# Optimization experiments

Hardware: AMD Instinct MI355X
Metric: run time of the kernel (lower is better)

## Reference

```python
import jax, jax.numpy as jnp
import numpy as np

T, B = 21, 4096
H, E, V = 1024, 50, 96
PAD = 0


def setup_inputs() -> dict:
    key = jax.random.key(0)
    ks = jax.random.split(key, 10)
    s_e = 1.0 / np.sqrt(H)  # torch LSTM init scale
    emb = jax.random.normal(ks[0], (V, E), jnp.float32)
    emb = emb.at[PAD].set(0.0)  # padding_idx row is zero
    return {
        "input_ids": jax.random.randint(ks[1], (T, B), 0, V),
        "h0": jax.random.normal(ks[2], (1, B, H), jnp.float32),
        "c0": jax.random.normal(ks[3], (1, B, H), jnp.float32),
        "emb": emb,
        "W_ih": jax.random.uniform(ks[4], (4 * H, E), jnp.float32, -s_e, s_e),
        "W_hh": jax.random.uniform(ks[5], (4 * H, H), jnp.float32, -s_e, s_e),
        "b_ih": jax.random.uniform(ks[6], (4 * H,), jnp.float32, -s_e, s_e),
        "b_hh": jax.random.uniform(ks[7], (4 * H,), jnp.float32, -s_e, s_e),
        "W_out": jax.random.uniform(ks[8], (V, H), jnp.float32, -s_e, s_e),
        "b_out": jax.random.uniform(ks[9], (V,), jnp.float32, -s_e, s_e),
    }


def reference(input_ids, h0, c0, emb, W_ih, W_hh, b_ih, b_hh, W_out, b_out):
    # char_embeds: (T, B, E)
    x = emb[input_ids]
    # Precompute input projections for all timesteps in one GEMM: (T, B, 4H)
    x_proj = jnp.einsum("tbe,ge->tbg", x, W_ih) + b_ih + b_hh

    def step(carry, xp_t):
        h, c = carry  # (B, H) each
        gates = xp_t + h @ W_hh.T  # (B, 4H), torch gate order i,f,g,o
        i, f, g, o = jnp.split(gates, 4, axis=-1)
        i = jax.nn.sigmoid(i)
        f = jax.nn.sigmoid(f)
        g = jnp.tanh(g)
        o = jax.nn.sigmoid(o)
        c = f * c + i * g
        h = o * jnp.tanh(c)
        return (h, c), h

    (h_T, c_T), h_ts = jax.lax.scan(step, (h0[0], c0[0]), x_proj)
    # char_output_projection: (T, B, V)
    scores = jnp.einsum("tbh,vh->tbv", h_ts, W_out) + b_out
    return scores, (h_T[None], c_T[None])
```

## Files before the change

kernel.cpp:

```cpp
#include <hip/hip_runtime.h>
#include <hip/hip_bf16.h>


#define T_STEPS 21
#define BSZ 4096
#define HDIM 1024
#define VOCAB 96
#define EDIM 50

typedef __attribute__((ext_vector_type(8))) short short8;
typedef __attribute__((ext_vector_type(4))) short shortx4;
typedef __attribute__((ext_vector_type(4))) float f32x4;

#define GLL16(g, l)                                                        \
  __builtin_amdgcn_global_load_lds(                                        \
      (const __attribute__((address_space(1))) void*)(g),                  \
      (__attribute__((address_space(3))) void*)(l), 16, 0, 0)

#define ASM_BARRIER() asm volatile("s_barrier" ::: "memory")
#define ASM_VMCNT3() asm volatile("s_waitcnt vmcnt(3)" ::: "memory")
#define ASM_VMCNT0() asm volatile("s_waitcnt vmcnt(0)" ::: "memory")

__device__ __forceinline__ float sigmoidf_fast(float x) {
  return 1.0f / (1.0f + __expf(-x));
}
__device__ __forceinline__ float tanhf_fast(float x) {
  return 2.0f / (1.0f + __expf(-2.0f * x)) - 1.0f;
}
__device__ __forceinline__ float b2f(short s) {
  return __uint_as_float(((unsigned int)(unsigned short)s) << 16);
}

__global__ void prep_convert(const float* __restrict__ Whh_f,
                             const float* __restrict__ Wout_f,
                             const float* __restrict__ h0,
                             __hip_bfloat16* __restrict__ Whh,
                             __hip_bfloat16* __restrict__ Wout,
                             __hip_bfloat16* __restrict__ hb0) {
  int idx = blockIdx.x * 256 + threadIdx.x;
  if (idx < 4 * HDIM * HDIM) {
    Whh[idx] = __float2bfloat16(Whh_f[idx]);
    hb0[idx] = __float2bfloat16(h0[idx]);
  }
  if (idx < VOCAB * HDIM) Wout[idx] = __float2bfloat16(Wout_f[idx]);
}

__global__ void prep_ptable(const float* __restrict__ emb,
                            const float* __restrict__ Wih,
                            const float* __restrict__ bih,
                            const float* __restrict__ bhh,
                            __hip_bfloat16* __restrict__ Pb) {
  int idx = blockIdx.x * 256 + threadIdx.x;
  int v = idx >> 12, g = idx & 4095;
  int gate = g >> 10, j = g & 1023;
  const float* er = emb + v * EDIM;
  const float* wr = Wih + g * EDIM;
  float s = bih[g] + bhh[g];
#pragma unroll 10
  for (int e = 0; e < EDIM; ++e) s += er[e] * wr[e];
  Pb[(size_t)(j >> 5) * 12288 + v * 128 + (j & 31) * 4 + gate] =
      __float2bfloat16(s);
}


#define TILE(kk, CB, SB, DOSTAGE, VMW)                                      \
  {                                                                         \
    const __hip_bfloat16* bufE =                                            \
        (const __hip_bfloat16*)(smem + (CB) * 24576);                       \
    short8 af[4], bf[4];                                                    \
    _Pragma("unroll") for (int mi = 0; mi < 4; ++mi)                        \
        af[mi] = *(const short8*)&bufE[a_off[mi]];                          \
    _Pragma("unroll") for (int g = 0; g < 4; ++g)                           \
        bf[g] = *(const short8*)&bufE[b_off[g]];                            \
    if (DOSTAGE) {                                                          \
      GLL16(hprev + aSrc[0] + ((kk) + 2) * 32,                              \
            smem + (SB) * 24576 + aDstB0);                                  \
      GLL16(hprev + aSrc[1] + ((kk) + 2) * 32,                              \
            smem + (SB) * 24576 + aDstB1);                                  \
      GLL16(Whh + bSrcE + ((kk) + 2) * 32, smem + (SB) * 24576 + bDstB);    \
    }                                                                       \
    ASM_BARRIER();                                                          \
    __builtin_amdgcn_s_setprio(1);                                          \
    _Pragma("unroll") for (int mi = 0; mi < 4; ++mi)                        \
        _Pragma("unroll") for (int g = 0; g < 4; ++g)                       \
            acc[mi][g] = __builtin_amdgcn_mfma_f32_16x16x32_bf16(           \
                af[mi], bf[g], acc[mi][g], 0, 0, 0);                        \
    __builtin_amdgcn_s_setprio(0);                                          \
    VMW;                                                                    \
    ASM_BARRIER();                                                          \
  }

template <bool LAST>
__global__ __launch_bounds__(512, 4) void lstm_step_kernel(
    const int* __restrict__ ids,
    const __hip_bfloat16* __restrict__ hprev,
    const __hip_bfloat16* __restrict__ Whh,
    const __hip_bfloat16* __restrict__ Pb,
    const float* __restrict__ c_in,
    float* __restrict__ c_out,
    __hip_bfloat16* __restrict__ hnext,
    float* __restrict__ hf32)
{
  __shared__ __align__(16) char smem[73728];

  const int tid = threadIdx.x;
  const int wid = tid >> 6;
  const int lane = tid & 63;
  const int wr = wid >> 1;
  const int wc = wid & 1;
  const int u16 = lane & 15;
  const int k16q = lane >> 4;

  const int bid = blockIdx.x;
  const int mt = (bid & 7) * 2 + ((bid >> 3) & 1);
  const int jt = bid >> 4;
  const int m0 = mt * 256;

  int a_off[4], b_off[4];
  {
    const int S = ((u16 & 1) << 2) | k16q;
#pragma unroll
    for (int mi = 0; mi < 4; ++mi) {
      const int La = wr * 32 + mi * 8 + (u16 >> 1);
      a_off[mi] = La * 64 + (S ^ (La & 7)) * 8;
    }
#pragma unroll
    for (int g = 0; g < 4; ++g) {
      const int Lb = wc * 32 + g * 8 + (u16 >> 1);
      b_off[g] = 8192 + Lb * 64 + (S ^ (Lb & 7)) * 8;
    }
  }

  size_t aSrc[2];
  size_t bSrcE;
  const int aDstB0 = wid * 2048;
  const int aDstB1 = wid * 2048 + 1024;
  const int bDstB = 16384 + wid * 1024;
  {
    const int Sp = lane & 7;
#pragma unroll
    for (int i = 0; i < 2; ++i) {
      const int La = wid * 16 + i * 8 + (lane >> 3);
      const int S = Sp ^ (La & 7);
      const int mrow = 2 * La + (S >> 2);
      aSrc[i] = (size_t)(m0 + mrow) * HDIM + (S & 3) * 8;
    }
    const int Lb = wid * 8 + (lane >> 3);
    const int S = Sp ^ (Lb & 7);
    const int n = 2 * Lb + (S >> 2);
    const int wcg = n >> 6, gate = (n >> 4) & 3, u = n & 15;
    bSrcE = (size_t)(gate * HDIM + jt * 32 + wcg * 16 + u) * HDIM +
            (S & 3) * 8;
  }

  GLL16(hprev + aSrc[0], smem + aDstB0);
  GLL16(hprev + aSrc[1], smem + aDstB1);
  GLL16(Whh + bSrcE, smem + bDstB);
  GLL16(hprev + aSrc[0] + 32, smem + 24576 + aDstB0);
  GLL16(hprev + aSrc[1] + 32, smem + 24576 + aDstB1);
  GLL16(Whh + bSrcE + 32, smem + 24576 + bDstB);
  ASM_VMCNT3();
  ASM_BARRIER();

  f32x4 acc[4][4] = {};

#pragma unroll 1
  for (int kb = 0; kb < 30; kb += 3) {
    TILE(kb, 0, 2, true, ASM_VMCNT3());
    TILE(kb + 1, 1, 0, true, ASM_VMCNT3());
    TILE(kb + 2, 2, 1, true, ASM_VMCNT3());
  }
  TILE(30, 0, 2, false, ASM_VMCNT0());
  TILE(31, 1, 0, false, {});

  const int jcol = jt * 32 + wc * 16 + u16;
  float cpre[4][4];
#pragma unroll
  for (int mi = 0; mi < 4; ++mi)
#pragma unroll
    for (int r = 0; r < 4; ++r)
      cpre[mi][r] = c_in[(size_t)(m0 + wr * 64 + mi * 16 + k16q * 4 + r) *
                             HDIM +
                         jcol];

  {
    const __hip_bfloat16* Pbj = Pb + (size_t)jt * 12288;
#pragma unroll
    for (int i = 0; i < 3; ++i)
      GLL16(Pbj + (wid * 3 + i) * 512 + lane * 8,
            smem + (wid * 3 + i) * 1024);
  }
  ASM_VMCNT0();
  ASM_BARRIER();

  const __hip_bfloat16* sPb = (const __hip_bfloat16*)smem;
  const int uo4 = (wc * 16 + u16) * 4;
  const int rb = m0 + wr * 64 + k16q * 4;
#pragma unroll
  for (int mi = 0; mi < 4; ++mi) {
#pragma unroll
    for (int r = 0; r < 4; ++r) {
      const int row = rb + mi * 16 + r;
      const int id = ids[row];
      const shortx4 pv = *(const shortx4*)&sPb[id * 128 + uo4];
      float iv = acc[mi][0][r] + b2f(pv[0]);
      float fv = acc[mi][1][r] + b2f(pv[1]);
      float gv = acc[mi][2][r] + b2f(pv[2]);
      float ov = acc[mi][3][r] + b2f(pv[3]);
      iv = sigmoidf_fast(iv);
      fv = sigmoidf_fast(fv);
      gv = tanhf_fast(gv);
      ov = sigmoidf_fast(ov);
      const size_t off = (size_t)row * HDIM + jcol;
      const float cc = fv * cpre[mi][r] + iv * gv;
      c_out[off] = cc;
      const float hh = ov * tanhf_fast(cc);
      hnext[off] = __float2bfloat16(hh);
      if (LAST) hf32[off] = hh;
    }
  }
}

__global__ __launch_bounds__(256, 2) void scores_kernel(
    const __hip_bfloat16* __restrict__ h,
    const __hip_bfloat16* __restrict__ Wout,
    const float* __restrict__ bout,
    float* __restrict__ out)
{
  __shared__ __align__(16) __hip_bfloat16 sA[128 * 128];
  __shared__ __align__(16) __hip_bfloat16 sB[96 * 128];

  const int tid = threadIdx.x;
  const int wave = tid >> 6, lane = tid & 63;
  const int u16 = lane & 15, k16q = lane >> 4;
  const long r0 = (long)blockIdx.x * 128;

  f32x4 acc[2][6] = {};

  const int srow4 = lane >> 4;
  const int sslot = lane & 15;

  for (int k0 = 0; k0 < HDIM; k0 += 128) {
#pragma unroll
    for (int i = 0; i < 8; ++i) {
      int row = wave * 32 + i * 4 + srow4;
      int gg = sslot ^ (row & 15);
      GLL16(h + (r0 + row) * HDIM + k0 + gg * 8,
            &sA[(wave * 32 + i * 4) * 128]);
    }
#pragma unroll
    for (int i = 0; i < 6; ++i) {
      int row = wave * 24 + i * 4 + srow4;
      int gg = sslot ^ (row & 15);
      GLL16(Wout + (size_t)row * HDIM + k0 + gg * 8,
            &sB[(wave * 24 + i * 4) * 128]);
    }
    __syncthreads();
#pragma unroll
    for (int kk = 0; kk < 128; kk += 32) {
      const int sl = (((kk >> 3) + k16q) ^ u16) * 8;
      short8 af[2], bf[6];
#pragma unroll
      for (int mi = 0; mi < 2; ++mi)
        af[mi] = *(const short8*)&sA[(wave * 32 + mi * 16 + u16) * 128 + sl];
#pragma unroll
      for (int ni = 0; ni < 6; ++ni)
        bf[ni] = *(const short8*)&sB[(ni * 16 + u16) * 128 + sl];
#pragma unroll
      for (int mi = 0; mi < 2; ++mi)
#pragma unroll
        for (int ni = 0; ni < 6; ++ni)
          acc[mi][ni] = __builtin_amdgcn_mfma_f32_16x16x32_bf16(
              af[mi], bf[ni], acc[mi][ni], 0, 0, 0);
    }
    __syncthreads();
  }

#pragma unroll
  for (int ni = 0; ni < 6; ++ni) {
    int v = ni * 16 + u16;
    float bv = bout[v];
#pragma unroll
    for (int mi = 0; mi < 2; ++mi)
#pragma unroll
      for (int r = 0; r < 4; ++r) {
        long grow = r0 + wave * 32 + mi * 16 + k16q * 4 + r;
        out[grow * VOCAB + v] = acc[mi][ni][r] + bv;
      }
  }
}

extern "C" void kernel_launch(void* const* d_in, const int* in_sizes, int n_in,
                              void* d_out, int out_size, void* d_ws,
                              size_t ws_size, hipStream_t stream) {
  const int* ids = (const int*)d_in[0];
  const float* h0 = (const float*)d_in[1];
  const float* c0 = (const float*)d_in[2];
  const float* emb = (const float*)d_in[3];
  const float* Wih = (const float*)d_in[4];
  const float* Whh_f = (const float*)d_in[5];
  const float* bih = (const float*)d_in[6];
  const float* bhh = (const float*)d_in[7];
  const float* Wout_f = (const float*)d_in[8];
  const float* bout = (const float*)d_in[9];

  float* out = (float*)d_out;
  float* scores = out;
  float* hT = out + (size_t)T_STEPS * BSZ * VOCAB;
  float* cT = hT + (size_t)BSZ * HDIM;

  const size_t BH = (size_t)BSZ * HDIM;
  char* w = (char*)d_ws;
  __hip_bfloat16* Pb = (__hip_bfloat16*)w;   w += (size_t)32 * 12288 * 2;
  __hip_bfloat16* Whh = (__hip_bfloat16*)w;  w += (size_t)4 * HDIM * HDIM * 2;
  __hip_bfloat16* Wout = (__hip_bfloat16*)w; w += (size_t)VOCAB * HDIM * 2;
  __hip_bfloat16* hts = (__hip_bfloat16*)w;
  size_t base = (size_t)32 * 12288 * 2 + (size_t)4 * HDIM * HDIM * 2 +
                (size_t)VOCAB * HDIM * 2;
  const bool full = ws_size >= base + (size_t)(T_STEPS + 1) * BH * 2;

  prep_convert<<<dim3((4 * HDIM * HDIM + 255) / 256), dim3(256), 0, stream>>>(
      Whh_f, Wout_f, h0, Whh, Wout, hts);
  prep_ptable<<<dim3((VOCAB * 4096) / 256), dim3(256), 0, stream>>>(
      emb, Wih, bih, bhh, Pb);

  for (int t = 0; t < T_STEPS; ++t) {
    __hip_bfloat16* hp = hts + (full ? (size_t)t * BH : (size_t)(t & 1) * BH);
    __hip_bfloat16* hn =
        hts + (full ? (size_t)(t + 1) * BH : (size_t)((t + 1) & 1) * BH);
    const float* cin = (t == 0) ? c0 : cT;
    if (t == T_STEPS - 1) {
      lstm_step_kernel<true><<<dim3(512), dim3(512), 0, stream>>>(
          ids + (size_t)t * BSZ, hp, Whh, Pb, cin, cT, hn, hT);
    } else {
      lstm_step_kernel<false><<<dim3(512), dim3(512), 0, stream>>>(
          ids + (size_t)t * BSZ, hp, Whh, Pb, cin, cT, hn, nullptr);
    }
    if (!full) {
      scores_kernel<<<dim3(BSZ / 128), dim3(256), 0, stream>>>(
          hn, Wout, bout, scores + (size_t)t * BSZ * VOCAB);
    }
  }
  if (full) {
    scores_kernel<<<dim3(T_STEPS * BSZ / 128), dim3(256), 0, stream>>>(
        hts + BH, Wout, bout, scores);
  }
}
```

Before: 1.170 ms.

## Double LSTM step tile width to 256x256 and restructure the barrier schedule

```diff
diff --git a/kernel.cpp b/kernel.cpp
--- a/kernel.cpp
+++ b/kernel.cpp
@@ -18,7 +18,7 @@
       (__attribute__((address_space(3))) void*)(l), 16, 0, 0)
 
 #define ASM_BARRIER() asm volatile("s_barrier" ::: "memory")
-#define ASM_VMCNT3() asm volatile("s_waitcnt vmcnt(3)" ::: "memory")
+#define ASM_VMCNT4() asm volatile("s_waitcnt vmcnt(4)" ::: "memory")
 #define ASM_VMCNT0() asm volatile("s_waitcnt vmcnt(0)" ::: "memory")
 
 __device__ __forceinline__ float sigmoidf_fast(float x) {
@@ -58,40 +58,42 @@
   float s = bih[g] + bhh[g];
 #pragma unroll 10
   for (int e = 0; e < EDIM; ++e) s += er[e] * wr[e];
-  Pb[(size_t)(j >> 5) * 12288 + v * 128 + (j & 31) * 4 + gate] =
+  Pb[(size_t)(j >> 6) * 24576 + v * 256 + (j & 63) * 4 + gate] =
       __float2bfloat16(s);
 }
 
 
-#define TILE(kk, CB, SB, DOSTAGE, VMW)                                      \
-  {                                                                         \
-    const __hip_bfloat16* bufE =                                            \
-        (const __hip_bfloat16*)(smem + (CB) * 24576);                       \
-    short8 af[4], bf[4];                                                    \
-    _Pragma("unroll") for (int mi = 0; mi < 4; ++mi)                        \
-        af[mi] = *(const short8*)&bufE[a_off[mi]];                          \
-    _Pragma("unroll") for (int g = 0; g < 4; ++g)                           \
-        bf[g] = *(const short8*)&bufE[b_off[g]];                            \
-    if (DOSTAGE) {                                                          \
-      GLL16(hprev + aSrc[0] + ((kk) + 2) * 32,                              \
-            smem + (SB) * 24576 + aDstB0);                                  \
-      GLL16(hprev + aSrc[1] + ((kk) + 2) * 32,                              \
-            smem + (SB) * 24576 + aDstB1);                                  \
-      GLL16(Whh + bSrcE + ((kk) + 2) * 32, smem + (SB) * 24576 + bDstB);    \
-    }                                                                       \
-    ASM_BARRIER();                                                          \
-    __builtin_amdgcn_s_setprio(1);                                          \
-    _Pragma("unroll") for (int mi = 0; mi < 4; ++mi)                        \
-        _Pragma("unroll") for (int g = 0; g < 4; ++g)                       \
-            acc[mi][g] = __builtin_amdgcn_mfma_f32_16x16x32_bf16(           \
-                af[mi], bf[g], acc[mi][g], 0, 0, 0);                        \
-    __builtin_amdgcn_s_setprio(0);                                          \
-    VMW;                                                                    \
-    ASM_BARRIER();                                                          \
+#define TILE(kk, CB, SB, DOSTAGE, VMW)                                     \
+  {                                                                        \
+    ASM_BARRIER();                                                         \
+    const __hip_bfloat16* bufE =                                           \
+        (const __hip_bfloat16*)(smem + (CB) * 32768);                      \
+    short8 af[8], bf[4];                                                   \
+    _Pragma("unroll") for (int mi = 0; mi < 8; ++mi)                       \
+        af[mi] = *(const short8*)&bufE[a_off[mi]];                         \
+    _Pragma("unroll") for (int g = 0; g < 4; ++g)                          \
+        bf[g] = *(const short8*)&bufE[b_off[g]];                           \
+    if (DOSTAGE) {                                                         \
+      GLL16(hprev + aSrc[0] + ((kk) + 2) * 32,                             \
+            smem + (SB) * 32768 + aDst0);                                  \
+      GLL16(hprev + aSrc[1] + ((kk) + 2) * 32,                             \
+            smem + (SB) * 32768 + aDst1);                                  \
+      GLL16(Whh + bSrc[0] + ((kk) + 2) * 32,                               \
+            smem + (SB) * 32768 + bDst0);                                  \
+      GLL16(Whh + bSrc[1] + ((kk) + 2) * 32,                               \
+            smem + (SB) * 32768 + bDst1);                                  \
+    }                                                                      \
+    __builtin_amdgcn_s_setprio(1);                                         \
+    _Pragma("unroll") for (int mi = 0; mi < 8; ++mi)                       \
+        _Pragma("unroll") for (int g = 0; g < 4; ++g)                      \
+            acc[mi][g] = __builtin_amdgcn_mfma_f32_16x16x32_bf16(          \
+                af[mi], bf[g], acc[mi][g], 0, 0, 0);                       \
+    __builtin_amdgcn_s_setprio(0);                                         \
+    VMW;                                                                   \
   }
 
 template <bool LAST>
-__global__ __launch_bounds__(512, 4) void lstm_step_kernel(
+__global__ __launch_bounds__(512, 2) void lstm_step_kernel(
     const int* __restrict__ ids,
     const __hip_bfloat16* __restrict__ hprev,
     const __hip_bfloat16* __restrict__ Whh,
@@ -101,13 +103,13 @@
     __hip_bfloat16* __restrict__ hnext,
     float* __restrict__ hf32)
 {
-  __shared__ __align__(16) char smem[73728];
+  __shared__ __align__(16) char smem[98304];
 
   const int tid = threadIdx.x;
   const int wid = tid >> 6;
   const int lane = tid & 63;
-  const int wr = wid >> 1;
-  const int wc = wid & 1;
+  const int wr = wid >> 2;
+  const int wc = wid & 3;
   const int u16 = lane & 15;
   const int k16q = lane >> 4;
 
@@ -116,12 +118,12 @@
   const int jt = bid >> 4;
   const int m0 = mt * 256;
 
-  int a_off[4], b_off[4];
+  int a_off[8], b_off[4];
   {
     const int S = ((u16 & 1) << 2) | k16q;
 #pragma unroll
-    for (int mi = 0; mi < 4; ++mi) {
-      const int La = wr * 32 + mi * 8 + (u16 >> 1);
+    for (int mi = 0; mi < 8; ++mi) {
+      const int La = wr * 64 + mi * 8 + (u16 >> 1);
       a_off[mi] = La * 64 + (S ^ (La & 7)) * 8;
     }
 #pragma unroll
@@ -131,78 +133,81 @@
     }
   }
 
-  size_t aSrc[2];
-  size_t bSrcE;
-  const int aDstB0 = wid * 2048;
-  const int aDstB1 = wid * 2048 + 1024;
-  const int bDstB = 16384 + wid * 1024;
+  size_t aSrc[2], bSrc[2];
+  const int aDst0 = wid * 2048;
+  const int aDst1 = wid * 2048 + 1024;
+  const int bDst0 = 16384 + wid * 2048;
+  const int bDst1 = 16384 + wid * 2048 + 1024;
   {
+    const int lrow = lane >> 3;
     const int Sp = lane & 7;
 #pragma unroll
-    for (int i = 0; i < 2; ++i) {
-      const int La = wid * 16 + i * 8 + (lane >> 3);
+    for (int q = 0; q < 2; ++q) {
+      const int La = wid * 16 + q * 8 + lrow;
       const int S = Sp ^ (La & 7);
-      const int mrow = 2 * La + (S >> 2);
-      aSrc[i] = (size_t)(m0 + mrow) * HDIM + (S & 3) * 8;
-    }
-    const int Lb = wid * 8 + (lane >> 3);
-    const int S = Sp ^ (Lb & 7);
-    const int n = 2 * Lb + (S >> 2);
-    const int wcg = n >> 6, gate = (n >> 4) & 3, u = n & 15;
-    bSrcE = (size_t)(gate * HDIM + jt * 32 + wcg * 16 + u) * HDIM +
-            (S & 3) * 8;
-  }
-
-  GLL16(hprev + aSrc[0], smem + aDstB0);
-  GLL16(hprev + aSrc[1], smem + aDstB1);
-  GLL16(Whh + bSrcE, smem + bDstB);
-  GLL16(hprev + aSrc[0] + 32, smem + 24576 + aDstB0);
-  GLL16(hprev + aSrc[1] + 32, smem + 24576 + aDstB1);
-  GLL16(Whh + bSrcE + 32, smem + 24576 + bDstB);
-  ASM_VMCNT3();
-  ASM_BARRIER();
-
-  f32x4 acc[4][4] = {};
+      const int arow = 2 * La + (S >> 2);
+      aSrc[q] = (size_t)(m0 + arow) * HDIM + (S & 3) * 8;
+      const int Lb = wid * 16 + q * 8 + lrow;
+      const int S2 = Sp ^ (Lb & 7);
+      const int n = 2 * Lb + (S2 >> 2);
+      const int q4 = n >> 6, gate = (n >> 4) & 3, u = n & 15;
+      bSrc[q] = (size_t)(gate * HDIM + jt * 64 + q4 * 16 + u) * HDIM +
+                (S2 & 3) * 8;
+    }
+  }
+
+  GLL16(hprev + aSrc[0], smem + aDst0);
+  GLL16(hprev + aSrc[1], smem + aDst1);
+  GLL16(Whh + bSrc[0], smem + bDst0);
+  GLL16(Whh + bSrc[1], smem + bDst1);
+  GLL16(hprev + aSrc[0] + 32, smem + 32768 + aDst0);
+  GLL16(hprev + aSrc[1] + 32, smem + 32768 + aDst1);
+  GLL16(Whh + bSrc[0] + 32, smem + 32768 + bDst0);
+  GLL16(Whh + bSrc[1] + 32, smem + 32768 + bDst1);
+  ASM_VMCNT4();
+
+  f32x4 acc[8][4] = {};
 
 #pragma unroll 1
   for (int kb = 0; kb < 30; kb += 3) {
-    TILE(kb, 0, 2, true, ASM_VMCNT3());
-    TILE(kb + 1, 1, 0, true, ASM_VMCNT3());
-    TILE(kb + 2, 2, 1, true, ASM_VMCNT3());
-  }
-  TILE(30, 0, 2, false, ASM_VMCNT0());
+    TILE(kb, 0, 2, true, ASM_VMCNT4());
+    TILE(kb + 1, 1, 0, true, ASM_VMCNT4());
+    TILE(kb + 2, 2, 1, true, ASM_VMCNT4());
+  }
+  TILE(30, 0, 0, false, ASM_VMCNT0());
   TILE(31, 1, 0, false, {});
-
-  const int jcol = jt * 32 + wc * 16 + u16;
-  float cpre[4][4];
-#pragma unroll
-  for (int mi = 0; mi < 4; ++mi)
+  ASM_BARRIER();
+
+  const int jcol = jt * 64 + wc * 16 + u16;
+  float cpre[8][4];
+#pragma unroll
+  for (int mi = 0; mi < 8; ++mi)
 #pragma unroll
     for (int r = 0; r < 4; ++r)
-      cpre[mi][r] = c_in[(size_t)(m0 + wr * 64 + mi * 16 + k16q * 4 + r) *
+      cpre[mi][r] = c_in[(size_t)(m0 + wr * 128 + mi * 16 + k16q * 4 + r) *
                              HDIM +
                          jcol];
 
   {
-    const __hip_bfloat16* Pbj = Pb + (size_t)jt * 12288;
-#pragma unroll
-    for (int i = 0; i < 3; ++i)
-      GLL16(Pbj + (wid * 3 + i) * 512 + lane * 8,
-            smem + (wid * 3 + i) * 1024);
+    const __hip_bfloat16* Pbj = Pb + (size_t)jt * 24576;
+#pragma unroll
+    for (int i = 0; i < 6; ++i)
+      GLL16(Pbj + (wid * 6 + i) * 512 + lane * 8,
+            smem + (wid * 6 + i) * 1024);
   }
   ASM_VMCNT0();
   ASM_BARRIER();
 
   const __hip_bfloat16* sPb = (const __hip_bfloat16*)smem;
   const int uo4 = (wc * 16 + u16) * 4;
-  const int rb = m0 + wr * 64 + k16q * 4;
-#pragma unroll
-  for (int mi = 0; mi < 4; ++mi) {
+  const int rb = m0 + wr * 128 + k16q * 4;
+#pragma unroll
+  for (int mi = 0; mi < 8; ++mi) {
 #pragma unroll
     for (int r = 0; r < 4; ++r) {
       const int row = rb + mi * 16 + r;
       const int id = ids[row];
-      const shortx4 pv = *(const shortx4*)&sPb[id * 128 + uo4];
+      const shortx4 pv = *(const shortx4*)&sPb[id * 256 + uo4];
       float iv = acc[mi][0][r] + b2f(pv[0]);
       float fv = acc[mi][1][r] + b2f(pv[1]);
       float gv = acc[mi][2][r] + b2f(pv[2]);
@@ -311,11 +316,11 @@
 
   const size_t BH = (size_t)BSZ * HDIM;
   char* w = (char*)d_ws;
-  __hip_bfloat16* Pb = (__hip_bfloat16*)w;   w += (size_t)32 * 12288 * 2;
+  __hip_bfloat16* Pb = (__hip_bfloat16*)w;   w += (size_t)16 * 24576 * 2;
   __hip_bfloat16* Whh = (__hip_bfloat16*)w;  w += (size_t)4 * HDIM * HDIM * 2;
   __hip_bfloat16* Wout = (__hip_bfloat16*)w; w += (size_t)VOCAB * HDIM * 2;
   __hip_bfloat16* hts = (__hip_bfloat16*)w;
-  size_t base = (size_t)32 * 12288 * 2 + (size_t)4 * HDIM * HDIM * 2 +
+  size_t base = (size_t)16 * 24576 * 2 + (size_t)4 * HDIM * HDIM * 2 +
                 (size_t)VOCAB * HDIM * 2;
   const bool full = ws_size >= base + (size_t)(T_STEPS + 1) * BH * 2;
 
@@ -330,10 +335,10 @@
         hts + (full ? (size_t)(t + 1) * BH : (size_t)((t + 1) & 1) * BH);
     const float* cin = (t == 0) ? c0 : cT;
     if (t == T_STEPS - 1) {
-      lstm_step_kernel<true><<<dim3(512), dim3(512), 0, stream>>>(
+      lstm_step_kernel<true><<<dim3(256), dim3(512), 0, stream>>>(
           ids + (size_t)t * BSZ, hp, Whh, Pb, cin, cT, hn, hT);
     } else {
-      lstm_step_kernel<false><<<dim3(512), dim3(512), 0, stream>>>(
+      lstm_step_kernel<false><<<dim3(256), dim3(512), 0, stream>>>(
           ids + (size_t)t * BSZ, hp, Whh, Pb, cin, cT, hn, nullptr);
     }
     if (!full) {
```

After: 1.094 ms. 6.5% less time.
